# Kernel tuning notes

Hardware: AMD Instinct MI355X
Metric: run time of the kernel (lower is better)

Reference implementation:

```python
import jax, jax.numpy as jnp
import numpy as np

B, TD, ND, FD, H = 16384, 256, 256, 512, 8
HID = [512, 256]


def _ln(x, g, b, eps=1e-5):
    m = jnp.mean(x, -1, keepdims=True)
    v = jnp.mean((x - m) ** 2, -1, keepdims=True)
    return (x - m) * jax.lax.rsqrt(v + eps) * g + b


def _mha1(q_in, k_in, v_in, wq, bq, wk, bk, wv, bv, wo, bo):
    # MultiheadAttention with seq_len=1 on both sides; eval mode (dropout off).
    Bq, E = q_in.shape
    dh = E // H
    q = (q_in @ wq.T + bq).reshape(Bq, H, dh)
    k = (k_in @ wk.T + bk).reshape(Bq, H, dh)
    scores = jnp.sum(q * k, -1) / np.sqrt(dh)          # [B, H]
    w = jax.nn.softmax(scores[..., None], axis=-1)      # [B, H, 1] -> exactly 1 (single key)
    attn = jnp.mean(w, axis=1)[:, None, :]              # averaged over heads -> [B, 1, 1]
    v = v_in @ wv.T + bv                                # attn weight == 1, so attn_out == v
    out = v @ wo.T + bo
    return out, attn


def setup_inputs():
    key = jax.random.key(0)
    ks = iter(jax.random.split(key, 40))
    def p(*shape):
        return jax.random.normal(next(ks), shape, dtype=jnp.float32) * 0.02
    inp = {
        'text_emb': jax.random.normal(next(ks), (B, TD), dtype=jnp.float32),
        'num_emb': jax.random.normal(next(ks), (B, ND), dtype=jnp.float32),
        'tp_w': p(FD, TD), 'tp_b': p(FD),
        'np_w': p(FD, ND), 'np_b': p(FD),
        'a1_wq': p(FD, FD), 'a1_wk': p(FD, FD), 'a1_wv': p(FD, FD),
        'a1_bq': p(FD), 'a1_bk': p(FD), 'a1_bv': p(FD),
        'a1_wo': p(FD, FD), 'a1_bo': p(FD),
        'a2_wq': p(FD, FD), 'a2_wk': p(FD, FD), 'a2_wv': p(FD, FD),
        'a2_bq': p(FD), 'a2_bk': p(FD), 'a2_bv': p(FD),
        'a2_wo': p(FD, FD), 'a2_bo': p(FD),
        'n1_g': jnp.ones((FD,), jnp.float32), 'n1_b': jnp.zeros((FD,), jnp.float32),
        'n2_g': jnp.ones((FD,), jnp.float32), 'n2_b': jnp.zeros((FD,), jnp.float32),
        'g_w': p(FD, 2 * FD), 'g_b': p(FD),
        'm1_w': p(HID[0], 2 * FD), 'm1_b': p(HID[0]),
        'ln1_g': jnp.ones((HID[0],), jnp.float32), 'ln1_b': jnp.zeros((HID[0],), jnp.float32),
        'm2_w': p(HID[1], HID[0]), 'm2_b': p(HID[1]),
        'ln2_g': jnp.ones((HID[1],), jnp.float32), 'ln2_b': jnp.zeros((HID[1],), jnp.float32),
    }
    return inp


def reference(text_emb, num_emb, tp_w, tp_b, np_w, np_b,
              a1_wq, a1_wk, a1_wv, a1_bq, a1_bk, a1_bv, a1_wo, a1_bo,
              a2_wq, a2_wk, a2_wv, a2_bq, a2_bk, a2_bv, a2_wo, a2_bo,
              n1_g, n1_b, n2_g, n2_b, g_w, g_b,
              m1_w, m1_b, ln1_g, ln1_b, m2_w, m2_b, ln2_g, ln2_b):
    t = text_emb @ tp_w.T + tp_b                        # [B, FD]
    n = num_emb @ np_w.T + np_b                         # [B, FD]
    n2t, attn_n2t = _mha1(n, t, t, a1_wq, a1_bq, a1_wk, a1_bk, a1_wv, a1_bv, a1_wo, a1_bo)
    n2t = _ln(n + n2t, n1_g, n1_b)
    t2n, attn_t2n = _mha1(t, n, n, a2_wq, a2_bq, a2_wk, a2_bk, a2_wv, a2_bv, a2_wo, a2_bo)
    t2n = _ln(t + t2n, n2_g, n2_b)
    comb = jnp.concatenate([n2t, t2n], axis=-1)         # [B, 2*FD]
    gate = jax.nn.sigmoid(comb @ g_w.T + g_b)           # [B, FD]
    h = jax.nn.gelu(_ln(comb @ m1_w.T + m1_b, ln1_g, ln1_b), approximate=False)
    fused = jax.nn.gelu(_ln(h @ m2_w.T + m2_b, ln2_g, ln2_b), approximate=False)
    return fused, gate, attn_n2t, attn_t2n
```

## Files before the change

kernel.cpp:

```cpp
#include <hip/hip_runtime.h>
#include <math.h>

typedef unsigned short u16;
typedef __bf16 bf16x8 __attribute__((ext_vector_type(8)));
typedef float f32x4 __attribute__((ext_vector_type(4)));
typedef short s16x8 __attribute__((ext_vector_type(8)));
typedef short s16x4 __attribute__((ext_vector_type(4)));

__device__ __forceinline__ float b2f(u16 u) {
    union { unsigned i; float f; } c; c.i = ((unsigned)u) << 16; return c.f;
}
__device__ __forceinline__ u16 f2b(float f) {
    union { float f; unsigned i; } c; c.f = f;
    return (u16)((c.i + 0x7fffu + ((c.i >> 16) & 1u)) >> 16);
}
__device__ __forceinline__ float gelu_f(float v) {
    return 0.5f * v * (1.0f + erff(v * 0.70710678118654752f));
}
__device__ __forceinline__ void async_cp16(const u16* g, u16* l) {
    __builtin_amdgcn_global_load_lds((const __attribute__((address_space(1))) void*)g,
                                     (__attribute__((address_space(3))) void*)l, 16, 0, 0);
}

template<int SUBN>
__global__ __launch_bounds__(256, 2)
void gemm_bt(const u16* __restrict__ A0, const u16* __restrict__ A1,
             const u16* __restrict__ W0, const u16* __restrict__ W1,
             const float* __restrict__ B0, const float* __restrict__ B1,
             const float* __restrict__ LG0, const float* __restrict__ LB0,
             const float* __restrict__ LG1, const float* __restrict__ LB1,
             void* __restrict__ O0v, void* __restrict__ O1v,
             int lda, int K, int halfBlocks, int ldo0, int ldo1,
             int mode0, int mode1)
{
    constexpr int NCOL = 256 * SUBN;
    constexpr int WCH  = NCOL / 64;
    constexpr int BUFE = (64 + NCOL) * 32;
    constexpr int EPIW = NCOL + 8;
    constexpr int EPIS = 64 * EPIW;
    __shared__ u16 sm[(2 * BUFE > EPIS) ? 2 * BUFE : EPIS];

    const int bx = blockIdx.x, by = blockIdx.y;
    const int half = (bx >= halfBlocks) ? 1 : 0;
    const int bxl = bx - half * halfBlocks;
    const u16* A = (half ? A1 : A0) + (size_t)by * 64 * lda;
    const u16* W = (half ? W1 : W0) + (size_t)bxl * NCOL * K;
    const float* bias = half ? B1 : B0;
    const float* lng = half ? LG1 : LG0;
    const float* lnb = half ? LB1 : LB0;
    void* outv = half ? O1v : O0v;
    const int ldo = half ? ldo1 : ldo0;
    const int mode = half ? mode1 : mode0;

    const int tid = threadIdx.x;
    const int lane = tid & 63;
    const int wave = tid >> 6;
    const int fc = lane & 15;
    const int quad = lane >> 4;

    int arw, ac8;
    { const int hi = tid >> 3, t7 = ((tid & 7) - hi) & 7; arw = (hi << 1) + (t7 >> 2); ac8 = t7 & 3; }
    int wrw[WCH], wc8[WCH];
#pragma unroll
    for (int c = 0; c < WCH; ++c) {
        const int p = tid + 256 * c;
        const int hi = p >> 3, t7 = ((p & 7) - hi) & 7;
        wrw[c] = (hi << 1) + (t7 >> 2); wc8[c] = t7 & 3;
    }

    int aoff[4];
#pragma unroll
    for (int i = 0; i < 4; ++i) {
        const int ar = i * 16 + fc;
        const int s = ((ar >> 1) << 3) + ((((ar & 1) << 2) + quad + (ar >> 1)) & 7);
        aoff[i] = s * 8;
    }
    int woff[4 * SUBN];
#pragma unroll
    for (int sub = 0; sub < SUBN; ++sub)
#pragma unroll
    for (int j = 0; j < 4; ++j) {
        const int wr = wave * (64 * SUBN) + sub * 64 + j * 16 + fc;
        const int s = ((wr >> 1) << 3) + ((((wr & 1) << 2) + quad + (wr >> 1)) & 7);
        woff[sub * 4 + j] = s * 8;
    }

    f32x4 acc[4][4 * SUBN];
#pragma unroll
    for (int i = 0; i < 4; ++i)
#pragma unroll
        for (int j = 0; j < 4 * SUBN; ++j)
            acc[i][j] = f32x4{0.f, 0.f, 0.f, 0.f};

    auto STAGE = [&](int b, int k0) {
        u16* base = sm + b * BUFE;
        async_cp16(A + (size_t)arw * lda + k0 + ac8 * 8, base + tid * 8);
#pragma unroll
        for (int c = 0; c < WCH; ++c)
            async_cp16(W + (size_t)wrw[c] * K + k0 + wc8[c] * 8,
                       base + 64 * 32 + (tid + 256 * c) * 8);
    };
    auto COMPUTE = [&](int b) {
        const u16* bA = sm + b * BUFE;
        const u16* bW = bA + 64 * 32;
        bf16x8 af[4];
#pragma unroll
        for (int i = 0; i < 4; ++i) af[i] = *(const bf16x8*)&bA[aoff[i]];
#pragma unroll
        for (int sub = 0; sub < SUBN; ++sub) {
            bf16x8 wf[4];
#pragma unroll
            for (int j = 0; j < 4; ++j) wf[j] = *(const bf16x8*)&bW[woff[sub * 4 + j]];
#pragma unroll
            for (int i = 0; i < 4; ++i)
#pragma unroll
            for (int j = 0; j < 4; ++j)
                acc[i][sub * 4 + j] =
                    __builtin_amdgcn_mfma_f32_16x16x32_bf16(af[i], wf[j], acc[i][sub * 4 + j], 0, 0, 0);
        }
    };

    const int NT = K >> 5;
    STAGE(0, 0);
    __syncthreads();
    int cur = 0;
    for (int t = 0; t < NT - 1; ++t) {
        STAGE(cur ^ 1, (t + 1) << 5);
        COMPUTE(cur);
        __syncthreads();
        cur ^= 1;
    }
    COMPUTE(cur);

    const int colb = bxl * NCOL;

    if (mode <= 1) {
#pragma unroll
        for (int sub = 0; sub < SUBN; ++sub)
#pragma unroll
        for (int j = 0; j < 4; ++j) {
            const int colh = colb + wave * 64 * SUBN + sub * 64 + j * 16 + fc;
            const float bv = bias[colh];
#pragma unroll
            for (int i = 0; i < 4; ++i)
#pragma unroll
            for (int r = 0; r < 4; ++r) {
                const int row = by * 64 + i * 16 + quad * 4 + r;
                const float v = acc[i][sub * 4 + j][r] + bv;
                if (mode == 1)
                    ((float*)outv)[(size_t)row * ldo + colh] = 1.0f / (1.0f + expf(-v));
                else
                    ((u16*)outv)[(size_t)row * ldo + colh] = f2b(v);
            }
        }
    } else {
        __syncthreads();
        float bb[SUBN * 4];
#pragma unroll
        for (int sub = 0; sub < SUBN; ++sub)
#pragma unroll
        for (int j = 0; j < 4; ++j)
            bb[sub * 4 + j] = bias[colb + wave * 64 * SUBN + sub * 64 + j * 16 + fc];
#pragma unroll
        for (int sub = 0; sub < SUBN; ++sub)
#pragma unroll
        for (int j = 0; j < 4; ++j) {
            const int col = wave * 64 * SUBN + sub * 64 + j * 16 + fc;
#pragma unroll
            for (int i = 0; i < 4; ++i)
#pragma unroll
            for (int r = 0; r < 4; ++r)
                sm[(i * 16 + quad * 4 + r) * EPIW + col] =
                    f2b(acc[i][sub * 4 + j][r] + bb[sub * 4 + j]);
        }
        __syncthreads();

        constexpr int CE = NCOL / 64;
        constexpr float INV = 1.0f / (float)NCOL;
        float gv[CE], bvv[CE];
#pragma unroll
        for (int e = 0; e < CE; ++e) {
            gv[e] = lng[lane * CE + e];
            bvv[e] = lnb[lane * CE + e];
        }
        for (int rr = 0; rr < 16; ++rr) {
            const int rl = wave * 16 + rr;
            const int grow = by * 64 + rl;
            float x[CE], s = 0.f, ss = 0.f;
            if constexpr (CE == 8) {
                s16x8 xv = *(const s16x8*)&sm[rl * EPIW + lane * 8];
#pragma unroll
                for (int e = 0; e < 8; ++e) { x[e] = b2f((u16)xv[e]); s += x[e]; ss += x[e] * x[e]; }
            } else {
                s16x4 xv = *(const s16x4*)&sm[rl * EPIW + lane * 4];
#pragma unroll
                for (int e = 0; e < 4; ++e) { x[e] = b2f((u16)xv[e]); s += x[e]; ss += x[e] * x[e]; }
            }
#pragma unroll
            for (int m = 32; m >= 1; m >>= 1) { s += __shfl_xor(s, m, 64); ss += __shfl_xor(ss, m, 64); }
            const float mean = s * INV;
            const float var = ss * INV - mean * mean;
            const float rs = rsqrtf(var + 1e-5f);
            float y[CE];
#pragma unroll
            for (int e = 0; e < CE; ++e) {
                y[e] = (x[e] - mean) * rs * gv[e] + bvv[e];
                if (mode >= 3) y[e] = gelu_f(y[e]);
            }
            if (mode == 4) {
                float* o = (float*)outv;
#pragma unroll
                for (int e = 0; e < CE; ++e)
                    o[(size_t)grow * ldo + colb + lane * CE + e] = y[e];
                if (lane == 0) {
                    o[(size_t)16384 * 768 + grow] = 1.0f;
                    o[(size_t)16384 * 769 + grow] = 1.0f;
                }
            } else {
                u16* o = (u16*)outv;
                if constexpr (CE == 8) {
                    s16x8 ov;
#pragma unroll
                    for (int e = 0; e < 8; ++e) ov[e] = (short)f2b(y[e]);
                    *(s16x8*)&o[(size_t)grow * ldo + colb + lane * 8] = ov;
                } else {
                    s16x4 ov;
#pragma unroll
                    for (int e = 0; e < 4; ++e) ov[e] = (short)f2b(y[e]);
                    *(s16x4*)&o[(size_t)grow * ldo + colb + lane * 4] = ov;
                }
            }
        }
    }
}


__device__ __forceinline__ void cvt_quads(const float* __restrict__ src,
                                          u16* __restrict__ dst, int bi, int tid)
{
#pragma unroll
    for (int c = 0; c < 2; ++c) {
        const int q = bi * 512 + tid + 256 * c;
        f32x4 v = *(const f32x4*)(src + (size_t)q * 4);
        s16x4 o;
        o[0] = (short)f2b(v[0]); o[1] = (short)f2b(v[1]);
        o[2] = (short)f2b(v[2]); o[3] = (short)f2b(v[3]);
        *(s16x4*)(dst + (size_t)q * 4) = o;
    }
}

__device__ void transpose_cvt64(const float* __restrict__ src, int C,
                                u16* __restrict__ dst, int R,
                                int tr, int tc, int tid, float* sm)
{
    const int lr = tid >> 4, lc4 = (tid & 15) * 4;
#pragma unroll
    for (int m = 0; m < 4; ++m) {
        const int i = lr + m * 16;
        f32x4 v = *(const f32x4*)&src[(size_t)(tr + i) * C + tc + lc4];
#pragma unroll
        for (int mm = 0; mm < 4; ++mm) sm[i * 65 + lc4 + mm] = v[mm];
    }
    __syncthreads();
#pragma unroll
    for (int m = 0; m < 4; ++m) {
        const int j = lr + m * 16;
        s16x4 o;
#pragma unroll
        for (int mm = 0; mm < 4; ++mm)
            o[mm] = (short)f2b(sm[(size_t)(lc4 + mm) * 65 + j]);
        *(s16x4*)&dst[(size_t)(tc + j) * R + tr + lc4] = o;
    }
}

__device__ void matvec_rows(const float* __restrict__ M, const float* __restrict__ v,
                            const float* __restrict__ add1, const float* __restrict__ add2,
                            float* __restrict__ out, int r0, int tid, float* sm)
{
    for (int i = tid; i < 512; i += 256) sm[i] = v[i];
    __syncthreads();
    const int row = r0 + (tid & 63), q = tid >> 6;
    float s = 0.f;
    for (int k = q * 128; k < q * 128 + 128; k += 4) {
        f32x4 m = *(const f32x4*)&M[(size_t)row * 512 + k];
        s += m[0] * sm[k] + m[1] * sm[k + 1] + m[2] * sm[k + 2] + m[3] * sm[k + 3];
    }
    sm[512 + tid] = s;
    __syncthreads();
    if (tid < 64)
        out[r0 + tid] = sm[512 + tid] + sm[512 + tid + 64] + sm[512 + tid + 128] +
                        sm[512 + tid + 192] + add1[r0 + tid] + add2[r0 + tid];
}

__global__ __launch_bounds__(256)
void prep_cvt(const float* __restrict__ text, const float* __restrict__ num,
              const float* __restrict__ tp_w, const float* __restrict__ np_w,
              const float* __restrict__ g_w, const float* __restrict__ m1_w,
              const float* __restrict__ m2_w,
              const float* __restrict__ a1_wv, const float* __restrict__ a2_wv,
              const float* __restrict__ a1_wo, const float* __restrict__ a2_wo,
              const float* __restrict__ a1_bv, const float* __restrict__ a1_bo,
              const float* __restrict__ a2_bv, const float* __restrict__ a2_bo,
              const float* __restrict__ tp_b, const float* __restrict__ np_b,
              u16* __restrict__ EMBc, u16* __restrict__ Wbig,
              u16* __restrict__ g_bf, u16* __restrict__ m1_bf, u16* __restrict__ m2_bf,
              u16* __restrict__ a1_wvT, u16* __restrict__ a2_wvT,
              u16* __restrict__ tp_wT, u16* __restrict__ np_wT,
              u16* __restrict__ a1_wo_bf, u16* __restrict__ a2_wo_bf,
              float* __restrict__ w1, float* __restrict__ w2,
              float* __restrict__ zb)
{
    __shared__ float smem[64 * 65];
    const int b = blockIdx.x, tid = threadIdx.x;
    if (b < 4096) {
#pragma unroll
        for (int c = 0; c < 2; ++c) {
            const int q = b * 512 + tid + 256 * c;
            const int e = q * 4, row = e >> 9, col = e & 511;
            const float* src = (col < 256) ? text + (size_t)row * 256 + col
                                           : num + (size_t)row * 256 + (col - 256);
            f32x4 v = *(const f32x4*)src;
            s16x4 o;
            o[0] = (short)f2b(v[0]); o[1] = (short)f2b(v[1]);
            o[2] = (short)f2b(v[2]); o[3] = (short)f2b(v[3]);
            *(s16x4*)(EMBc + e) = o;
        }
    } else if (b < 4352) { cvt_quads(g_w, g_bf, b - 4096, tid); }
    else if (b < 4608) { cvt_quads(m1_w, m1_bf, b - 4352, tid); }
    else if (b < 4672) { cvt_quads(m2_w, m2_bf, b - 4608, tid); }
    else if (b < 4736) {
#pragma unroll
        for (int c = 0; c < 2; ++c) {
            const int q = (b - 4672) * 512 + tid + 256 * c;
            const int e = q * 4, row = e >> 8, col = e & 255;
            f32x4 v = *(const f32x4*)(np_w + e);
            s16x4 o;
            o[0] = (short)f2b(v[0]); o[1] = (short)f2b(v[1]);
            o[2] = (short)f2b(v[2]); o[3] = (short)f2b(v[3]);
            *(s16x4*)(Wbig + (size_t)row * 512 + 256 + col) = o;
        }
    } else if (b < 4800) {
#pragma unroll
        for (int c = 0; c < 2; ++c) {
            const int q = (b - 4736) * 512 + tid + 256 * c;
            const int e = q * 4, row = e >> 8, col = e & 255;
            f32x4 v = *(const f32x4*)(tp_w + e);
            s16x4 o;
            o[0] = (short)f2b(v[0]); o[1] = (short)f2b(v[1]);
            o[2] = (short)f2b(v[2]); o[3] = (short)f2b(v[3]);
            *(s16x4*)(Wbig + (size_t)(512 + row) * 512 + col) = o;
        }
    } else if (b < 4864) {
        const int t = b - 4800;
        transpose_cvt64(a1_wv, 512, a1_wvT, 512, (t >> 3) * 64, (t & 7) * 64, tid, smem);
    } else if (b < 4928) {
        const int t = b - 4864;
        transpose_cvt64(a2_wv, 512, a2_wvT, 512, (t >> 3) * 64, (t & 7) * 64, tid, smem);
    } else if (b < 4960) {
        const int t = b - 4928;
        transpose_cvt64(tp_w, 256, tp_wT, 512, (t >> 2) * 64, (t & 3) * 64, tid, smem);
    } else if (b < 4992) {
        const int t = b - 4960;
        transpose_cvt64(np_w, 256, np_wT, 512, (t >> 2) * 64, (t & 3) * 64, tid, smem);
    } else if (b < 5120) { cvt_quads(a1_wo, a1_wo_bf, b - 4992, tid); }
    else if (b < 5248) { cvt_quads(a2_wo, a2_wo_bf, b - 5120, tid); }
    else if (b < 5256) {
        matvec_rows(a1_wo, a1_bv, a1_bo, np_b, w1, (b - 5248) * 64, tid, smem);
    } else if (b < 5264) {
        matvec_rows(a2_wo, a2_bv, a2_bo, tp_b, w2, (b - 5256) * 64, tid, smem);
    } else {
        *(f32x4*)&zb[tid * 4] = f32x4{0.f, 0.f, 0.f, 0.f};
    }
}

__global__ __launch_bounds__(256)
void prep_bias(const u16* __restrict__ M1, const u16* __restrict__ M2,
               const float* __restrict__ tp_b, const float* __restrict__ np_b,
               const float* __restrict__ w1, const float* __restrict__ w2,
               float* __restrict__ bbig)
{
    __shared__ float sm[768];
    const int b = blockIdx.x, tid = threadIdx.x;
    const int side = b >> 3, r0 = (b & 7) * 64;
    const u16* M = side ? M2 : M1;
    const float* v = side ? np_b : tp_b;
    const float* w = side ? w2 : w1;
    float* out = bbig + side * 512;
    for (int i = tid; i < 512; i += 256) sm[i] = v[i];
    __syncthreads();
    const int row = r0 + (tid & 63), q = tid >> 6;
    float s = 0.f;
    for (int k = q * 128; k < q * 128 + 128; k += 8) {
        s16x8 m = *(const s16x8*)&M[(size_t)row * 512 + k];
#pragma unroll
        for (int j = 0; j < 8; ++j) s += b2f((u16)m[j]) * sm[k + j];
    }
    sm[512 + tid] = s;
    __syncthreads();
    if (tid < 64)
        out[r0 + tid] = sm[512 + tid] + sm[512 + tid + 64] + sm[512 + tid + 128] +
                        sm[512 + tid + 192] + w[r0 + tid];
}

extern "C" void kernel_launch(void* const* d_in, const int* in_sizes, int n_in,
                              void* d_out, int out_size, void* d_ws, size_t ws_size,
                              hipStream_t stream)
{
    const float* text  = (const float*)d_in[0];
    const float* num   = (const float*)d_in[1];
    const float* tp_w  = (const float*)d_in[2];
    const float* tp_b  = (const float*)d_in[3];
    const float* np_w  = (const float*)d_in[4];
    const float* np_b  = (const float*)d_in[5];
    const float* a1_wv = (const float*)d_in[8];
    const float* a1_bv = (const float*)d_in[11];
    const float* a1_wo = (const float*)d_in[12];
    const float* a1_bo = (const float*)d_in[13];
    const float* a2_wv = (const float*)d_in[16];
    const float* a2_bv = (const float*)d_in[19];
    const float* a2_wo = (const float*)d_in[20];
    const float* a2_bo = (const float*)d_in[21];
    const float* n1_g  = (const float*)d_in[22];
    const float* n1_b  = (const float*)d_in[23];
    const float* n2_g  = (const float*)d_in[24];
    const float* n2_b  = (const float*)d_in[25];
    const float* g_w   = (const float*)d_in[26];
    const float* g_b   = (const float*)d_in[27];
    const float* m1_w  = (const float*)d_in[28];
    const float* m1_b  = (const float*)d_in[29];
    const float* ln1_g = (const float*)d_in[30];
    const float* ln1_b = (const float*)d_in[31];
    const float* m2_w  = (const float*)d_in[32];
    const float* m2_b  = (const float*)d_in[33];
    const float* ln2_g = (const float*)d_in[34];
    const float* ln2_b = (const float*)d_in[35];

    float* outp = (float*)d_out;
    char* ob = (char*)d_out;
    char* ws = (char*)d_ws;
    const size_t KB = 1024, MB = 1048576;

    u16* Wbig    = (u16*)(ob);
    u16* g_bf    = (u16*)(ob + 1 * MB);
    u16* m1_bf   = (u16*)(ob + 2 * MB);
    u16* a1_wvT  = (u16*)(ob + 3 * MB + 256 * KB);
    u16* a2_wvT  = (u16*)(ob + 3 * MB + 768 * KB);
    u16* tp_wT   = (u16*)(ob + 4 * MB + 256 * KB);
    u16* np_wT   = (u16*)(ob + 4 * MB + 512 * KB);
    u16* a1_wo_bf= (u16*)(ob + 4 * MB + 768 * KB);
    u16* a2_wo_bf= (u16*)(ob + 5 * MB + 256 * KB);
    u16* M1      = (u16*)(ob + 5 * MB + 768 * KB);
    u16* M2      = (u16*)(ob + 6 * MB + 256 * KB);
    float* w1    = (float*)(ob + 6 * MB + 768 * KB);
    float* w2    = w1 + 512;
    float* bbig  = w1 + 1024;
    float* zb    = w1 + 2048;
    u16* EMBc    = (u16*)(ob + 16 * MB);
    u16* X     = (u16*)ws;
    u16* m2_bf = (u16*)(ws + 32 * MB);
    u16* h     = (u16*)(ws + 48 * MB);

    dim3 blk(256);

    prep_cvt<<<5265, blk, 0, stream>>>(text, num, tp_w, np_w, g_w, m1_w, m2_w,
        a1_wv, a2_wv, a1_wo, a2_wo, a1_bv, a1_bo, a2_bv, a2_bo, tp_b, np_b,
        EMBc, Wbig, g_bf, m1_bf, m2_bf, a1_wvT, a2_wvT, tp_wT, np_wT,
        a1_wo_bf, a2_wo_bf, w1, w2, zb);
    gemm_bt<2><<<dim3(2, 8), blk, 0, stream>>>(a1_wo_bf, a2_wo_bf, a1_wvT, a2_wvT,
        zb, zb, nullptr, nullptr, nullptr, nullptr,
        M1, M2, 512, 512, 1, 512, 512, 0, 0);
    prep_bias<<<16, blk, 0, stream>>>(M1, M2, tp_b, np_b, w1, w2, bbig);
    gemm_bt<1><<<dim3(2, 8), blk, 0, stream>>>(M1, M2, tp_wT, np_wT,
        zb, zb, nullptr, nullptr, nullptr, nullptr,
        Wbig, Wbig + (size_t)512 * 512 + 256, 512, 512, 1, 512, 512, 0, 0);
    gemm_bt<2><<<dim3(2, 256), blk, 0, stream>>>(EMBc, EMBc,
        Wbig, Wbig + (size_t)512 * 512, bbig, bbig + 512,
        n1_g, n1_b, n2_g, n2_b,
        X, X + 512, 512, 512, 1, 1024, 1024, 2, 2);
    gemm_bt<2><<<dim3(2, 256), blk, 0, stream>>>(X, X, g_bf, m1_bf, g_b, m1_b,
        nullptr, nullptr, ln1_g, ln1_b,
        outp + (size_t)16384 * 256, h, 1024, 1024, 1, 512, 512, 1, 3);
    gemm_bt<1><<<dim3(1, 256), blk, 0, stream>>>(h, h, m2_bf, m2_bf, m2_b, m2_b,
        ln2_g, ln2_b, ln2_g, ln2_b,
        outp, outp, 512, 512, 1, 256, 256, 4, 4);
}
```

Before: 337.4 us.

## Halve GEMM row tile, single-buffer staging, and fuse LayerNorm in registers

Shrinks the GEMM M-tile from 64 to 32 rows and doubles the grid. It drops the double-buffered shared-memory pipeline in favour of a single buffer with two barriers per K step, and raises the launch bound to 4 blocks per CU. The LayerNorm epilogue now computes row statistics straight from the fp32 accumulators, using lane shuffles plus a small cross-wave shared-memory reduction, instead of round-tripping bf16 values through a large shared staging tile. The aim is higher occupancy and a cheaper epilogue. The cost is lost load/compute overlap, twice the weight-tile traffic per output row, and non-vectorised scalar output stores.

```diff
diff --git a/kernel.cpp b/kernel.cpp
--- a/kernel.cpp
+++ b/kernel.cpp
@@ -23,7 +23,7 @@
 }
 
 template<int SUBN>
-__global__ __launch_bounds__(256, 2)
+__global__ __launch_bounds__(256, 4)
 void gemm_bt(const u16* __restrict__ A0, const u16* __restrict__ A1,
              const u16* __restrict__ W0, const u16* __restrict__ W1,
              const float* __restrict__ B0, const float* __restrict__ B1,
@@ -35,15 +35,15 @@
 {
     constexpr int NCOL = 256 * SUBN;
     constexpr int WCH  = NCOL / 64;
-    constexpr int BUFE = (64 + NCOL) * 32;
-    constexpr int EPIW = NCOL + 8;
-    constexpr int EPIS = 64 * EPIW;
-    __shared__ u16 sm[(2 * BUFE > EPIS) ? 2 * BUFE : EPIS];
+    __shared__ u16 sA[32 * 32];
+    __shared__ u16 sW[NCOL * 32];
+    __shared__ float sp[4][32][2];
+    __shared__ float mrs[32][2];
 
     const int bx = blockIdx.x, by = blockIdx.y;
     const int half = (bx >= halfBlocks) ? 1 : 0;
     const int bxl = bx - half * halfBlocks;
-    const u16* A = (half ? A1 : A0) + (size_t)by * 64 * lda;
+    const u16* A = (half ? A1 : A0) + (size_t)by * 32 * lda;
     const u16* W = (half ? W1 : W0) + (size_t)bxl * NCOL * K;
     const float* bias = half ? B1 : B0;
     const float* lng = half ? LG1 : LG0;
@@ -68,9 +68,9 @@
         wrw[c] = (hi << 1) + (t7 >> 2); wc8[c] = t7 & 3;
     }
 
-    int aoff[4];
-#pragma unroll
-    for (int i = 0; i < 4; ++i) {
+    int aoff[2];
+#pragma unroll
+    for (int i = 0; i < 2; ++i) {
         const int ar = i * 16 + fc;
         const int s = ((ar >> 1) << 3) + ((((ar & 1) << 2) + quad + (ar >> 1)) & 7);
         aoff[i] = s * 8;
@@ -85,52 +85,41 @@
         woff[sub * 4 + j] = s * 8;
     }
 
-    f32x4 acc[4][4 * SUBN];
-#pragma unroll
-    for (int i = 0; i < 4; ++i)
+    f32x4 acc[2][4 * SUBN];
+#pragma unroll
+    for (int i = 0; i < 2; ++i)
 #pragma unroll
         for (int j = 0; j < 4 * SUBN; ++j)
             acc[i][j] = f32x4{0.f, 0.f, 0.f, 0.f};
 
-    auto STAGE = [&](int b, int k0) {
-        u16* base = sm + b * BUFE;
-        async_cp16(A + (size_t)arw * lda + k0 + ac8 * 8, base + tid * 8);
+    const int NT = K >> 5;
+    for (int t = 0; t < NT; ++t) {
+        const int k0 = t << 5;
+        if (tid < 128)
+            async_cp16(A + (size_t)arw * lda + k0 + ac8 * 8, &sA[tid * 8]);
 #pragma unroll
         for (int c = 0; c < WCH; ++c)
             async_cp16(W + (size_t)wrw[c] * K + k0 + wc8[c] * 8,
-                       base + 64 * 32 + (tid + 256 * c) * 8);
-    };
-    auto COMPUTE = [&](int b) {
-        const u16* bA = sm + b * BUFE;
-        const u16* bW = bA + 64 * 32;
-        bf16x8 af[4];
-#pragma unroll
-        for (int i = 0; i < 4; ++i) af[i] = *(const bf16x8*)&bA[aoff[i]];
+                       &sW[(tid + 256 * c) * 8]);
+        __syncthreads();
+
+        bf16x8 af[2];
+#pragma unroll
+        for (int i = 0; i < 2; ++i) af[i] = *(const bf16x8*)&sA[aoff[i]];
 #pragma unroll
         for (int sub = 0; sub < SUBN; ++sub) {
             bf16x8 wf[4];
 #pragma unroll
-            for (int j = 0; j < 4; ++j) wf[j] = *(const bf16x8*)&bW[woff[sub * 4 + j]];
-#pragma unroll
-            for (int i = 0; i < 4; ++i)
+            for (int j = 0; j < 4; ++j) wf[j] = *(const bf16x8*)&sW[woff[sub * 4 + j]];
+#pragma unroll
+            for (int i = 0; i < 2; ++i)
 #pragma unroll
             for (int j = 0; j < 4; ++j)
                 acc[i][sub * 4 + j] =
                     __builtin_amdgcn_mfma_f32_16x16x32_bf16(af[i], wf[j], acc[i][sub * 4 + j], 0, 0, 0);
         }
-    };
-
-    const int NT = K >> 5;
-    STAGE(0, 0);
-    __syncthreads();
-    int cur = 0;
-    for (int t = 0; t < NT - 1; ++t) {
-        STAGE(cur ^ 1, (t + 1) << 5);
-        COMPUTE(cur);
         __syncthreads();
-        cur ^= 1;
-    }
-    COMPUTE(cur);
+    }
 
     const int colb = bxl * NCOL;
 
@@ -142,10 +131,10 @@
             const int colh = colb + wave * 64 * SUBN + sub * 64 + j * 16 + fc;
             const float bv = bias[colh];
 #pragma unroll
-            for (int i = 0; i < 4; ++i)
+            for (int i = 0; i < 2; ++i)
 #pragma unroll
             for (int r = 0; r < 4; ++r) {
-                const int row = by * 64 + i * 16 + quad * 4 + r;
+                const int row = by * 32 + i * 16 + quad * 4 + r;
                 const float v = acc[i][sub * 4 + j][r] + bv;
                 if (mode == 1)
                     ((float*)outv)[(size_t)row * ldo + colh] = 1.0f / (1.0f + expf(-v));
@@ -154,82 +143,77 @@
             }
         }
     } else {
+        float gvv[SUBN * 4], bvv[SUBN * 4];
+#pragma unroll
+        for (int sub = 0; sub < SUBN; ++sub)
+#pragma unroll
+        for (int j = 0; j < 4; ++j) {
+            const int feat = wave * 64 * SUBN + sub * 64 + j * 16 + fc;
+            const float bv = bias[feat];
+            gvv[sub * 4 + j] = lng[feat];
+            bvv[sub * 4 + j] = lnb[feat];
+#pragma unroll
+            for (int i = 0; i < 2; ++i)
+#pragma unroll
+            for (int r = 0; r < 4; ++r)
+                acc[i][sub * 4 + j][r] += bv;
+        }
+#pragma unroll
+        for (int i = 0; i < 2; ++i)
+#pragma unroll
+        for (int r = 0; r < 4; ++r) {
+            float s = 0.f, ss = 0.f;
+#pragma unroll
+            for (int sj = 0; sj < SUBN * 4; ++sj) {
+                const float v = acc[i][sj][r];
+                s += v; ss += v * v;
+            }
+#pragma unroll
+            for (int m = 1; m <= 8; m <<= 1) {
+                s += __shfl_xor(s, m, 64);
+                ss += __shfl_xor(ss, m, 64);
+            }
+            if (fc == 0) {
+                const int rl = i * 16 + quad * 4 + r;
+                sp[wave][rl][0] = s;
+                sp[wave][rl][1] = ss;
+            }
+        }
         __syncthreads();
-        float bb[SUBN * 4];
-#pragma unroll
-        for (int sub = 0; sub < SUBN; ++sub)
-#pragma unroll
-        for (int j = 0; j < 4; ++j)
-            bb[sub * 4 + j] = bias[colb + wave * 64 * SUBN + sub * 64 + j * 16 + fc];
-#pragma unroll
-        for (int sub = 0; sub < SUBN; ++sub)
-#pragma unroll
-        for (int j = 0; j < 4; ++j) {
-            const int col = wave * 64 * SUBN + sub * 64 + j * 16 + fc;
-#pragma unroll
-            for (int i = 0; i < 4; ++i)
-#pragma unroll
-            for (int r = 0; r < 4; ++r)
-                sm[(i * 16 + quad * 4 + r) * EPIW + col] =
-                    f2b(acc[i][sub * 4 + j][r] + bb[sub * 4 + j]);
-        }
-        __syncthreads();
-
-        constexpr int CE = NCOL / 64;
         constexpr float INV = 1.0f / (float)NCOL;
-        float gv[CE], bvv[CE];
-#pragma unroll
-        for (int e = 0; e < CE; ++e) {
-            gv[e] = lng[lane * CE + e];
-            bvv[e] = lnb[lane * CE + e];
-        }
-        for (int rr = 0; rr < 16; ++rr) {
-            const int rl = wave * 16 + rr;
-            const int grow = by * 64 + rl;
-            float x[CE], s = 0.f, ss = 0.f;
-            if constexpr (CE == 8) {
-                s16x8 xv = *(const s16x8*)&sm[rl * EPIW + lane * 8];
-#pragma unroll
-                for (int e = 0; e < 8; ++e) { x[e] = b2f((u16)xv[e]); s += x[e]; ss += x[e] * x[e]; }
-            } else {
-                s16x4 xv = *(const s16x4*)&sm[rl * EPIW + lane * 4];
-#pragma unroll
-                for (int e = 0; e < 4; ++e) { x[e] = b2f((u16)xv[e]); s += x[e]; ss += x[e] * x[e]; }
-            }
-#pragma unroll
-            for (int m = 32; m >= 1; m >>= 1) { s += __shfl_xor(s, m, 64); ss += __shfl_xor(ss, m, 64); }
+        if (tid < 32) {
+            const float s  = sp[0][tid][0] + sp[1][tid][0] + sp[2][tid][0] + sp[3][tid][0];
+            const float ss = sp[0][tid][1] + sp[1][tid][1] + sp[2][tid][1] + sp[3][tid][1];
             const float mean = s * INV;
             const float var = ss * INV - mean * mean;
-            const float rs = rsqrtf(var + 1e-5f);
-            float y[CE];
-#pragma unroll
-            for (int e = 0; e < CE; ++e) {
-                y[e] = (x[e] - mean) * rs * gv[e] + bvv[e];
-                if (mode >= 3) y[e] = gelu_f(y[e]);
+            mrs[tid][0] = mean;
+            mrs[tid][1] = rsqrtf(var + 1e-5f);
+        }
+        __syncthreads();
+#pragma unroll
+        for (int i = 0; i < 2; ++i)
+#pragma unroll
+        for (int r = 0; r < 4; ++r) {
+            const int rl = i * 16 + quad * 4 + r;
+            const int grow = by * 32 + rl;
+            const float mean = mrs[rl][0], rs = mrs[rl][1];
+#pragma unroll
+            for (int sub = 0; sub < SUBN; ++sub)
+#pragma unroll
+            for (int j = 0; j < 4; ++j) {
+                const int feat = wave * 64 * SUBN + sub * 64 + j * 16 + fc;
+                float y = (acc[i][sub * 4 + j][r] - mean) * rs * gvv[sub * 4 + j] + bvv[sub * 4 + j];
+                if (mode >= 3) y = gelu_f(y);
+                if (mode == 4)
+                    ((float*)outv)[(size_t)grow * ldo + feat] = y;
+                else
+                    ((u16*)outv)[(size_t)grow * ldo + feat] = f2b(y);
             }
-            if (mode == 4) {
-                float* o = (float*)outv;
-#pragma unroll
-                for (int e = 0; e < CE; ++e)
-                    o[(size_t)grow * ldo + colb + lane * CE + e] = y[e];
-                if (lane == 0) {
-                    o[(size_t)16384 * 768 + grow] = 1.0f;
-                    o[(size_t)16384 * 769 + grow] = 1.0f;
-                }
-            } else {
-                u16* o = (u16*)outv;
-                if constexpr (CE == 8) {
-                    s16x8 ov;
-#pragma unroll
-                    for (int e = 0; e < 8; ++e) ov[e] = (short)f2b(y[e]);
-                    *(s16x8*)&o[(size_t)grow * ldo + colb + lane * 8] = ov;
-                } else {
-                    s16x4 ov;
-#pragma unroll
-                    for (int e = 0; e < 4; ++e) ov[e] = (short)f2b(y[e]);
-                    *(s16x4*)&o[(size_t)grow * ldo + colb + lane * 4] = ov;
-                }
-            }
+        }
+        if (mode == 4 && tid < 32) {
+            float* o = (float*)outv;
+            o[(size_t)16384 * 768 + by * 32 + tid] = 1.0f;
+            o[(size_t)16384 * 769 + by * 32 + tid] = 1.0f;
         }
     }
 }
@@ -466,21 +450,21 @@
         a1_wv, a2_wv, a1_wo, a2_wo, a1_bv, a1_bo, a2_bv, a2_bo, tp_b, np_b,
         EMBc, Wbig, g_bf, m1_bf, m2_bf, a1_wvT, a2_wvT, tp_wT, np_wT,
         a1_wo_bf, a2_wo_bf, w1, w2, zb);
-    gemm_bt<2><<<dim3(2, 8), blk, 0, stream>>>(a1_wo_bf, a2_wo_bf, a1_wvT, a2_wvT,
+    gemm_bt<2><<<dim3(2, 16), blk, 0, stream>>>(a1_wo_bf, a2_wo_bf, a1_wvT, a2_wvT,
         zb, zb, nullptr, nullptr, nullptr, nullptr,
         M1, M2, 512, 512, 1, 512, 512, 0, 0);
     prep_bias<<<16, blk, 0, stream>>>(M1, M2, tp_b, np_b, w1, w2, bbig);
-    gemm_bt<1><<<dim3(2, 8), blk, 0, stream>>>(M1, M2, tp_wT, np_wT,
+    gemm_bt<1><<<dim3(2, 16), blk, 0, stream>>>(M1, M2, tp_wT, np_wT,
         zb, zb, nullptr, nullptr, nullptr, nullptr,
         Wbig, Wbig + (size_t)512 * 512 + 256, 512, 512, 1, 512, 512, 0, 0);
-    gemm_bt<2><<<dim3(2, 256), blk, 0, stream>>>(EMBc, EMBc,
+    gemm_bt<2><<<dim3(2, 512), blk, 0, stream>>>(EMBc, EMBc,
         Wbig, Wbig + (size_t)512 * 512, bbig, bbig + 512,
         n1_g, n1_b, n2_g, n2_b,
         X, X + 512, 512, 512, 1, 1024, 1024, 2, 2);
-    gemm_bt<2><<<dim3(2, 256), blk, 0, stream>>>(X, X, g_bf, m1_bf, g_b, m1_b,
+    gemm_bt<2><<<dim3(2, 512), blk, 0, stream>>>(X, X, g_bf, m1_bf, g_b, m1_b,
         nullptr, nullptr, ln1_g, ln1_b,
         outp + (size_t)16384 * 256, h, 1024, 1024, 1, 512, 512, 1, 3);
-    gemm_bt<1><<<dim3(1, 256), blk, 0, stream>>>(h, h, m2_bf, m2_bf, m2_b, m2_b,
+    gemm_bt<1><<<dim3(1, 512), blk, 0, stream>>>(h, h, m2_bf, m2_bf, m2_b, m2_b,
         ln2_g, ln2_b, ln2_g, ln2_b,
         outp, outp, 512, 512, 1, 256, 256, 4, 4);
 }
```

New measurement: 416.0 us. 23.3% more time.
